# Performance work log

Hardware: AMD Instinct MI355X
Metric: run time of the kernel (lower is better)

The kernel has to match this reference:

```python
import jax, jax.numpy as jnp
import numpy as np


def setup_inputs() -> dict:
    key = jax.random.key(0)
    k1, k2 = jax.random.split(key)
    B, N1, N2 = 4, 8192, 8192
    pc1 = jax.random.normal(k1, (B, N1, 3), dtype=jnp.float32)
    pc2 = jax.random.normal(k2, (B, N2, 3), dtype=jnp.float32)
    return {"pc1": pc1, "pc2": pc2}


def reference(pc1, pc2):
    """Chamfer distance: CD(P,Q) = mean_p min_q ||p-q||^2 + mean_q min_p ||q-p||^2.

    pc1: (B, N1, 3), pc2: (B, N2, 3) -> (B,)
    Uses ||p-q||^2 = ||p||^2 + ||q||^2 - 2 p.q to avoid the (B,N1,N2,3)
    broadcasted-difference intermediate; only the (B,N1,N2) matrix is formed.
    """
    sq1 = jnp.sum(pc1 * pc1, axis=-1)                     # (B, N1)
    sq2 = jnp.sum(pc2 * pc2, axis=-1)                     # (B, N2)
    cross = jnp.einsum("bnd,bmd->bnm", pc1, pc2)          # (B, N1, N2)
    dist = sq1[:, :, None] + sq2[:, None, :] - 2.0 * cross  # (B, N1, N2)
    d12 = jnp.min(dist, axis=2).mean(axis=1)              # (B,) pc1 -> pc2
    d21 = jnp.min(dist, axis=1).mean(axis=1)              # (B,) pc2 -> pc1
    return d12 + d21
```

## Files before the change

kernel.cpp:

```cpp
#include <hip/hip_runtime.h>


typedef _Float16 half8  __attribute__((ext_vector_type(8)));
typedef float    f32x16 __attribute__((ext_vector_type(16)));

#define NPTS   8192
#define NB     4
#define SPLITS 4
#define TPW    64
#define QWIN   (TPW * 32)

#define MFMA_V(d, a, b, c)                                             \
    asm("v_mfma_f32_32x32x16_f16 %0, %1, %2, %3"                       \
        : "=&v"(d) : "v"(a), "v"(b), "v"(c))

__global__ __launch_bounds__(256, 3) void chamfer_main(
    const float* __restrict__ pc1, const float* __restrict__ pc2,
    float* __restrict__ ws_row)
{
    __shared__ half8 Bf[(TPW + 4) * 64];

    int bid = blockIdx.x;
    const int pt  = bid & 31;            bid >>= 5;
    const int qs  = bid & (SPLITS - 1);  bid >>= 2;
    const int b   = bid & (NB - 1);      bid >>= 2;
    const int dir = bid;

    const int tid = threadIdx.x;
    const int w = tid >> 6, lane = tid & 63;
    const int col = lane & 31, g = lane >> 5;
    const int pbase = pt * 256 + w * 64;

    const float* Acl = dir ? pc2 : pc1;
    const float* Bcl = dir ? pc1 : pc2;

    const _Float16 one = (_Float16)1.0f, zz = (_Float16)0.0f;

    for (int i = tid; i < QWIN; i += 256) {
        const int t = i >> 5, c = i & 31;
        const float* Q = Bcl + ((size_t)b * NPTS + qs * QWIN + i) * 3;
        const float qx = Q[0], qy = Q[1], qz = Q[2];

        const _Float16 hx = (_Float16)qx, hy = (_Float16)qy, hz = (_Float16)qz;
        const _Float16 lx = (_Float16)(qx - (float)hx);
        const _Float16 ly = (_Float16)(qy - (float)hy);
        const _Float16 lz = (_Float16)(qz - (float)hz);
        const float sq = fmaf(qx, qx, fmaf(qy, qy, qz * qz));
        const _Float16 sh = (_Float16)sq;
        const _Float16 sl = (_Float16)(sq - (float)sh);

        const _Float16 nhx = (_Float16)(-2.0f * (float)hx);
        const _Float16 nhy = (_Float16)(-2.0f * (float)hy);
        const _Float16 nhz = (_Float16)(-2.0f * (float)hz);
        const _Float16 nlx = (_Float16)(-2.0f * (float)lx);
        const _Float16 nly = (_Float16)(-2.0f * (float)ly);
        const _Float16 nlz = (_Float16)(-2.0f * (float)lz);

        Bf[t * 64 + c]      = (half8){nhx, nhy, nhz, nlx, nly, nlz, nhx, nhy};
        Bf[t * 64 + 32 + c] = (half8){nhz, one, one, sh,  sl,  zz,  zz,  zz};
    }

    half8 a0, a1;
    #pragma unroll
    for (int h = 0; h < 2; ++h) {
        const float* P = Acl + ((size_t)b * NPTS + pbase + h * 32 + col) * 3;
        const float px = P[0], py = P[1], pz = P[2];
        const _Float16 hx = (_Float16)px, hy = (_Float16)py, hz = (_Float16)pz;
        const _Float16 lx = (_Float16)(px - (float)hx);
        const _Float16 ly = (_Float16)(py - (float)hy);
        const _Float16 lz = (_Float16)(pz - (float)hz);
        const float sq1 = fmaf(px, px, fmaf(py, py, pz * pz));
        const _Float16 sh = (_Float16)sq1;
        const _Float16 sl = (_Float16)(sq1 - (float)sh);
        half8 a;
        if (g == 0) a = (half8){hx, hy, hz, hx, hy, hz, lx, ly};
        else        a = (half8){lz, sh, sl, one, one, zz, zz, zz};
        if (h == 0) a0 = a; else a1 = a;
    }

    f32x16 rowmin0, rowmin1;
    #pragma unroll
    for (int r = 0; r < 16; ++r) { rowmin0[r] = 3.402823466e+38f;
                                   rowmin1[r] = 3.402823466e+38f; }
    f32x16 zero16;
    #pragma unroll
    for (int r = 0; r < 16; ++r) zero16[r] = 0.0f;

    __syncthreads();

    half8 p0 = Bf[0 * 64 + lane], p1 = Bf[1 * 64 + lane];
    half8 p2 = Bf[2 * 64 + lane], p3 = Bf[3 * 64 + lane];

    #pragma unroll 4
    for (int t = 0; t < TPW; t += 2) {
        const half8 m0 = Bf[(t + 4) * 64 + lane];
        const half8 m1 = Bf[(t + 5) * 64 + lane];

        f32x16 acc00, acc01, acc10, acc11;
        MFMA_V(acc00, a0, p0, zero16);
        MFMA_V(acc01, a0, p1, zero16);
        MFMA_V(acc10, a1, p0, zero16);
        MFMA_V(acc11, a1, p1, zero16);

        __builtin_amdgcn_sched_barrier(0);
        asm volatile("s_nop 7\n\ts_nop 7");
        __builtin_amdgcn_sched_barrier(0);

        #pragma unroll
        for (int r = 0; r < 16; ++r)
            rowmin0[r] = fminf(fminf(acc00[r], acc01[r]), rowmin0[r]);
        #pragma unroll
        for (int r = 0; r < 16; ++r)
            rowmin1[r] = fminf(fminf(acc10[r], acc11[r]), rowmin1[r]);

        p0 = p2; p1 = p3; p2 = m0; p3 = m1;
    }

    const size_t obase = (((size_t)dir * NB + b) * SPLITS + qs) * NPTS + pbase;
    #pragma unroll
    for (int r = 0; r < 16; ++r) {
        float v = rowmin0[r];
        v = fminf(v, __shfl_xor(v, 1, 64));
        v = fminf(v, __shfl_xor(v, 2, 64));
        v = fminf(v, __shfl_xor(v, 4, 64));
        v = fminf(v, __shfl_xor(v, 8, 64));
        v = fminf(v, __shfl_xor(v, 16, 64));
        float u = rowmin1[r];
        u = fminf(u, __shfl_xor(u, 1, 64));
        u = fminf(u, __shfl_xor(u, 2, 64));
        u = fminf(u, __shfl_xor(u, 4, 64));
        u = fminf(u, __shfl_xor(u, 8, 64));
        u = fminf(u, __shfl_xor(u, 16, 64));
        if (col == 0) {
            const int row = (r & 3) + 8 * (r >> 2) + 4 * g;
            ws_row[obase + row]      = v;
            ws_row[obase + 32 + row] = u;
        }
    }
}

__global__ __launch_bounds__(256) void chamfer_reduce(
    const float* __restrict__ ws_row, float* __restrict__ partial)
{
    int bid = blockIdx.x;
    const int sl  = bid & 31; bid >>= 5;
    const int b   = bid & 3;  bid >>= 2;
    const int dir = bid;

    const int p = sl * 256 + threadIdx.x;
    const float* base = ws_row + (((size_t)dir * NB + b) * SPLITS) * NPTS + p;
    float sum = fminf(fminf(base[0],        base[NPTS]),
                      fminf(base[2 * NPTS], base[3 * NPTS]));

    for (int off = 32; off; off >>= 1) sum += __shfl_down(sum, off, 64);
    __shared__ float red[4];
    if (!(threadIdx.x & 63)) red[threadIdx.x >> 6] = sum;
    __syncthreads();
    if (!threadIdx.x)
        partial[blockIdx.x] = red[0] + red[1] + red[2] + red[3];
}

__global__ __launch_bounds__(64) void chamfer_final(
    const float* __restrict__ partial, float* __restrict__ out)
{
    const int b = blockIdx.x, t = threadIdx.x;
    const int dir = t >> 5, sl = t & 31;
    float v = partial[(((size_t)dir * NB + b) << 5) + sl];
    for (int off = 32; off; off >>= 1) v += __shfl_down(v, off, 64);
    if (!t) out[b] = v * (1.0f / (float)NPTS);
}

extern "C" void kernel_launch(void* const* d_in, const int* in_sizes, int n_in,
                              void* d_out, int out_size, void* d_ws, size_t ws_size,
                              hipStream_t stream)
{
    const float* pc1 = (const float*)d_in[0];
    const float* pc2 = (const float*)d_in[1];
    float* out = (float*)d_out;

    char* ws = (char*)d_ws;
    float* ws_row  = (float*)ws;
    float* partial = (float*)(ws + (1 << 20));

    chamfer_main<<<1024, 256, 0, stream>>>(pc1, pc2, ws_row);
    chamfer_reduce<<<256, 256, 0, stream>>>(ws_row, partial);
    chamfer_final<<<NB, 64, 0, stream>>>(partial, out);
}
```

Measured before the change: 33.64 us.

## Double query splits, use v_min3 and split MFMA groups for more occupancy

```diff
diff --git a/kernel.cpp b/kernel.cpp
--- a/kernel.cpp
+++ b/kernel.cpp
@@ -6,23 +6,27 @@
 
 #define NPTS   8192
 #define NB     4
-#define SPLITS 4
-#define TPW    64
+#define SPLITS 8
+#define TPW    32
 #define QWIN   (TPW * 32)
 
 #define MFMA_V(d, a, b, c)                                             \
     asm("v_mfma_f32_32x32x16_f16 %0, %1, %2, %3"                       \
         : "=&v"(d) : "v"(a), "v"(b), "v"(c))
 
-__global__ __launch_bounds__(256, 3) void chamfer_main(
+#define MIN3(dst, s0, s1)                                              \
+    asm("v_min3_f32 %0, %1, %2, %0"                                    \
+        : "+v"(dst) : "v"(s0), "v"(s1))
+
+__global__ __launch_bounds__(256, 4) void chamfer_main(
     const float* __restrict__ pc1, const float* __restrict__ pc2,
     float* __restrict__ ws_row)
 {
-    __shared__ half8 Bf[(TPW + 4) * 64];
+    __shared__ half8 Bf[(TPW + 2) * 64];
 
     int bid = blockIdx.x;
     const int pt  = bid & 31;            bid >>= 5;
-    const int qs  = bid & (SPLITS - 1);  bid >>= 2;
+    const int qs  = bid & (SPLITS - 1);  bid >>= 3;
     const int b   = bid & (NB - 1);      bid >>= 2;
     const int dir = bid;
 
@@ -78,10 +82,10 @@
         if (h == 0) a0 = a; else a1 = a;
     }
 
-    f32x16 rowmin0, rowmin1;
+    float rm0[16], rm1[16];
     #pragma unroll
-    for (int r = 0; r < 16; ++r) { rowmin0[r] = 3.402823466e+38f;
-                                   rowmin1[r] = 3.402823466e+38f; }
+    for (int r = 0; r < 16; ++r) { rm0[r] = 3.402823466e+38f;
+                                   rm1[r] = 3.402823466e+38f; }
     f32x16 zero16;
     #pragma unroll
     for (int r = 0; r < 16; ++r) zero16[r] = 0.0f;
@@ -89,47 +93,50 @@
     __syncthreads();
 
     half8 p0 = Bf[0 * 64 + lane], p1 = Bf[1 * 64 + lane];
-    half8 p2 = Bf[2 * 64 + lane], p3 = Bf[3 * 64 + lane];
 
-    #pragma unroll 4
+    #pragma unroll 2
     for (int t = 0; t < TPW; t += 2) {
-        const half8 m0 = Bf[(t + 4) * 64 + lane];
-        const half8 m1 = Bf[(t + 5) * 64 + lane];
+        const half8 n0 = Bf[(t + 2) * 64 + lane];
+        const half8 n1 = Bf[(t + 3) * 64 + lane];
 
-        f32x16 acc00, acc01, acc10, acc11;
-        MFMA_V(acc00, a0, p0, zero16);
-        MFMA_V(acc01, a0, p1, zero16);
-        MFMA_V(acc10, a1, p0, zero16);
-        MFMA_V(acc11, a1, p1, zero16);
+        {
+            f32x16 acc0, acc1;
+            MFMA_V(acc0, a0, p0, zero16);
+            MFMA_V(acc1, a0, p1, zero16);
+            __builtin_amdgcn_sched_barrier(0);
+            asm volatile("s_nop 7\n\ts_nop 7\n\ts_nop 3");
+            __builtin_amdgcn_sched_barrier(0);
+            #pragma unroll
+            for (int r = 0; r < 16; ++r) MIN3(rm0[r], acc0[r], acc1[r]);
+        }
+        {
+            f32x16 acc0, acc1;
+            MFMA_V(acc0, a1, p0, zero16);
+            MFMA_V(acc1, a1, p1, zero16);
+            __builtin_amdgcn_sched_barrier(0);
+            asm volatile("s_nop 7\n\ts_nop 7\n\ts_nop 3");
+            __builtin_amdgcn_sched_barrier(0);
+            #pragma unroll
+            for (int r = 0; r < 16; ++r) MIN3(rm1[r], acc0[r], acc1[r]);
+        }
 
-        __builtin_amdgcn_sched_barrier(0);
-        asm volatile("s_nop 7\n\ts_nop 7");
-        __builtin_amdgcn_sched_barrier(0);
-
-        #pragma unroll
-        for (int r = 0; r < 16; ++r)
-            rowmin0[r] = fminf(fminf(acc00[r], acc01[r]), rowmin0[r]);
-        #pragma unroll
-        for (int r = 0; r < 16; ++r)
-            rowmin1[r] = fminf(fminf(acc10[r], acc11[r]), rowmin1[r]);
-
-        p0 = p2; p1 = p3; p2 = m0; p3 = m1;
+        p0 = n0; p1 = n1;
     }
 
     const size_t obase = (((size_t)dir * NB + b) * SPLITS + qs) * NPTS + pbase;
     #pragma unroll
     for (int r = 0; r < 16; ++r) {
-        float v = rowmin0[r];
+        float v = rm0[r];
         v = fminf(v, __shfl_xor(v, 1, 64));
         v = fminf(v, __shfl_xor(v, 2, 64));
         v = fminf(v, __shfl_xor(v, 4, 64));
         v = fminf(v, __shfl_xor(v, 8, 64));
         v = fminf(v, __shfl_xor(v, 16, 64));
-        float u = rowmin1[r];
+        float u = rm1[r];
         u = fminf(u, __shfl_xor(u, 1, 64));
         u = fminf(u, __shfl_xor(u, 2, 64));
+        u = fminf(u, __shfl_xor(u, 8, 64));
         u = fminf(u, __shfl_xor(u, 4, 64));
-        u = fminf(u, __shfl_xor(u, 8, 64));
         u = fminf(u, __shfl_xor(u, 16, 64));
         if (col == 0) {
             const int row = (r & 3) + 8 * (r >> 2) + 4 * g;
@@ -149,8 +156,11 @@
 
     const int p = sl * 256 + threadIdx.x;
     const float* base = ws_row + (((size_t)dir * NB + b) * SPLITS) * NPTS + p;
-    float sum = fminf(fminf(base[0],        base[NPTS]),
-                      fminf(base[2 * NPTS], base[3 * NPTS]));
+    float m0 = fminf(base[0],            base[NPTS]);
+    float m1 = fminf(base[2 * NPTS],     base[3 * NPTS]);
+    float m2 = fminf(base[4 * NPTS],     base[5 * NPTS]);
+    float m3 = fminf(base[6 * NPTS],     base[7 * NPTS]);
+    float sum = fminf(fminf(m0, m1), fminf(m2, m3));
 
     for (int off = 32; off; off >>= 1) sum += __shfl_down(sum, off, 64);
     __shared__ float red[4];
@@ -180,9 +190,9 @@
 
     char* ws = (char*)d_ws;
     float* ws_row  = (float*)ws;
-    float* partial = (float*)(ws + (1 << 20));
+    float* partial = (float*)(ws + (2 << 20));
 
-    chamfer_main<<<1024, 256, 0, stream>>>(pc1, pc2, ws_row);
+    chamfer_main<<<2048, 256, 0, stream>>>(pc1, pc2, ws_row);
     chamfer_reduce<<<256, 256, 0, stream>>>(ws_row, partial);
     chamfer_final<<<NB, 64, 0, stream>>>(partial, out);
 }
```

Result: slower. 35.06 us (+4.2%).
